# Optimization experiments

Measured on AMD Instinct MI355X. Metric: run time of the kernel, lower is better.

The kernel has to match this reference:

```python
import jax, jax.numpy as jnp
import numpy as np

B, N, D = 16, 512, 12
HID, HEADS = 32, 4
C = HID // HEADS  # per-head channels = 8


def setup_inputs() -> dict:
    key = jax.random.key(0)
    ks = jax.random.split(key, 12)
    s = 0.1
    return {
        "x": jax.random.normal(ks[0], (B, N, D), dtype=jnp.float32),
        "adj": jax.random.randint(ks[1], (B, N, N), 0, 2, dtype=jnp.int32),
        # node_proj: Linear(D, HID)
        "Wp": jax.random.normal(ks[2], (HID, D), dtype=jnp.float32) * s,
        "bp": jax.random.normal(ks[3], (HID,), dtype=jnp.float32) * s,
        # GATConv lin: Linear(HID, HEADS*C, bias=False)
        "Wg": jax.random.normal(ks[4], (HEADS * C, HID), dtype=jnp.float32) * s,
        "att_src": jax.random.normal(ks[5], (HEADS, C), dtype=jnp.float32) * s,
        "att_dst": jax.random.normal(ks[6], (HEADS, C), dtype=jnp.float32) * s,
        "bias_g": jax.random.normal(ks[7], (HEADS * C,), dtype=jnp.float32) * s,
        # edge_mlp: Linear(2*HID, HID) -> ReLU -> Linear(HID, 1) -> Sigmoid
        "W1": jax.random.normal(ks[8], (HID, 2 * HID), dtype=jnp.float32) * s,
        "b1": jax.random.normal(ks[9], (HID,), dtype=jnp.float32) * s,
        "w2": jax.random.normal(ks[10], (HID,), dtype=jnp.float32) * s,
        "b2": jax.random.normal(ks[11], (1,), dtype=jnp.float32) * s,
    }


def reference(x, adj, Wp, bp, Wg, att_src, att_dst, bias_g, W1, b1, w2, b2):
    Bq, Nq, _ = x.shape
    adj_b = adj != 0
    eye = jnp.eye(Nq, dtype=bool)

    # node_proj + ReLU
    h = jax.nn.relu(jnp.einsum('bnd,hd->bnh', x, Wp) + bp)  # [B,N,HID]

    # GATConv (PyG semantics): messages flow src=i (row) -> dst=j (col),
    # self-loops removed then re-added => diagonal forced on.
    g = jnp.einsum('bnd,kd->bnk', h, Wg).reshape(Bq, Nq, HEADS, C)  # [B,N,H,C]
    a_s = jnp.einsum('bnhc,hc->bnh', g, att_src)  # [B,N,H]
    a_d = jnp.einsum('bnhc,hc->bnh', g, att_dst)  # [B,N,H]
    logits = jax.nn.leaky_relu(a_s[:, :, None, :] + a_d[:, None, :, :], 0.2)  # [B,i,j,H]
    mask_sl = adj_b | eye
    logits = jnp.where(mask_sl[..., None], logits, -1e9)
    alpha = jax.nn.softmax(logits, axis=1)  # softmax over source i per target j
    h_gnn = jnp.einsum('bijh,bihc->bjhc', alpha, g).reshape(Bq, Nq, HEADS * C) + bias_g

    # edge MLP on all (i,j) pairs: cat([h_i, h_j]) -> split W1
    W1i, W1j = W1[:, :HID], W1[:, HID:]
    ti = jnp.einsum('bnd,hd->bnh', h_gnn, W1i)  # [B,N,HID] (row / i part)
    tj = jnp.einsum('bnd,hd->bnh', h_gnn, W1j)  # [B,N,HID] (col / j part)
    hidden = jax.nn.relu(ti[:, :, None, :] + tj[:, None, :, :] + b1)  # [B,N,N,HID]
    score = jax.nn.sigmoid(jnp.einsum('bijh,h->bij', hidden, w2) + b2[0])

    out_mask = adj_b & ~eye
    return jnp.where(out_mask, score, jnp.float32(0.0))
```

## Files before the change

### kernel.cpp

```cpp
#include <hip/hip_runtime.h>
#include <cstdint>

#define Bq 16
#define Nq 512
#define Dq 12
#define HID 32
#define HEADS 4
#define Cq 8

#define OFF_G     0u
#define OFF_AS    262144u
#define OFF_AD    294912u
#define OFF_TIT   327680u
#define OFF_TJBT  589824u
#define OFF_PACK  851968u

__global__ __launch_bounds__(256) void k0_node(
    const float* __restrict__ x, const float* __restrict__ Wp, const float* __restrict__ bp,
    const float* __restrict__ Wg, const float* __restrict__ att_src,
    const float* __restrict__ att_dst, float* __restrict__ ws) {
    __shared__ float xs[8 * Dq];
    __shared__ float hs[8][HID];
    int n_sub = threadIdx.x >> 5;
    int k = threadIdx.x & 31;
    int node0 = blockIdx.x * 8;
    if (threadIdx.x < 8 * Dq) xs[threadIdx.x] = x[(size_t)node0 * Dq + threadIdx.x];
    __syncthreads();
    float s = bp[k];
#pragma unroll
    for (int d = 0; d < Dq; d++) s = fmaf(Wp[k * Dq + d], xs[n_sub * Dq + d], s);
    hs[n_sub][k] = s > 0.f ? s : 0.f;
    __syncthreads();
    float g = 0.f;
#pragma unroll
    for (int d = 0; d < HID; d++) g = fmaf(Wg[k * HID + d], hs[n_sub][d], g);
    int nid = node0 + n_sub;
    ws[OFF_G + (size_t)nid * HID + k] = g;
    float ss = g * att_src[k];
    float sd = g * att_dst[k];
#pragma unroll
    for (int off = 1; off < 8; off <<= 1) {
        ss += __shfl_xor(ss, off);
        sd += __shfl_xor(sd, off);
    }
    if ((k & 7) == 0) {
        int h = k >> 3;
        ws[OFF_AS + (size_t)nid * HEADS + h] = ss;
        ws[OFF_AD + (size_t)nid * HEADS + h] = sd;
    }
}

__global__ __launch_bounds__(256, 4) void k1_fused(
    const int* __restrict__ adj, const float* __restrict__ bias_g,
    const float* __restrict__ W1, const float* __restrict__ b1,
    float* __restrict__ ws) {
    int b = blockIdx.y;
    int j0 = blockIdx.x * 8;
    int t = threadIdx.x;
    int jl = t & 7;
    int ig = t >> 3;
    int par = ig >> 4;
    int j = j0 + jl;

    __shared__ float smem[5376];
    float* red = smem;
    float* hgs = smem + 1440;
    float* W1s = smem + 1728;
    float* tjs = smem + 3904;
    uint32_t* mskp = (uint32_t*)(smem + 5120);

    float4 adv = *(const float4*)(ws + OFF_AD + ((size_t)b * Nq + j) * HEADS);
    const float* Gb = ws + OFF_G + (size_t)b * Nq * HID;
    const float* Ab = ws + OFF_AS + (size_t)b * Nq * HEADS;
    int ii_s = t >> 2, q_s = t & 3;

    float4 ga, gb2;
    float av;
    {
        const float* src = Gb + (size_t)ii_s * HID + q_s * 8;
        ga = *(const float4*)src;
        gb2 = *(const float4*)(src + 4);
        av = Ab[t];
        *(float4*)&smem[ii_s * 36 + q_s * 8] = ga;
        *(float4*)&smem[ii_s * 36 + q_s * 8 + 4] = gb2;
        smem[4608 + t] = av;
    }
    const int* adjp = adj + ((size_t)b * Nq + ig) * Nq + j;
    int cur[2], nxt[2];
    cur[0] = adjp[0];
    cur[1] = adjp[(size_t)32 * Nq];

    float lsum[HEADS] = {0.f, 0.f, 0.f, 0.f};
    float acc[HEADS][Cq] = {};
    uint32_t mask = 0;

    for (int c = 0; c < 8; c++) {
        __syncthreads();
        const float* gsc = (c & 1) ? smem + 2304 : smem;
        const float* asc = (c & 1) ? smem + 4864 : smem + 4608;
        if (c < 7) {
            const float* src = Gb + (size_t)((c + 1) * 64 + ii_s) * HID + q_s * 8;
            ga = *(const float4*)src;
            gb2 = *(const float4*)(src + 4);
            av = Ab[(c + 1) * 256 + t];
            nxt[0] = adjp[(size_t)(64 * (c + 1)) * Nq];
            nxt[1] = adjp[(size_t)(64 * (c + 1) + 32) * Nq];
        }
#pragma unroll
        for (int kk = 0; kk < 2; kk++) {
            int i = 64 * c + 32 * kk + ig;
            int a = cur[kk];
            bool msk = (a != 0) || (i == j);
            mask |= (uint32_t)(a != 0) << (4 * c + 2 * kk + par);
            int ii = 32 * kk + ig;
            float4 asv = *(const float4*)&asc[ii * 4];
            const float* gr = &gsc[ii * 36];
            float zs[HEADS] = {asv.x + adv.x, asv.y + adv.y, asv.z + adv.z, asv.w + adv.w};
#pragma unroll
            for (int h = 0; h < HEADS; h++) {
                float z = zs[h];
                float lk = z > 0.f ? z : 0.2f * z;
                float e = msk ? __expf(lk) : 0.f;
                lsum[h] += e;
                float4 g0 = *(const float4*)(gr + h * 8);
                float4 g1 = *(const float4*)(gr + h * 8 + 4);
                acc[h][0] = fmaf(e, g0.x, acc[h][0]);
                acc[h][1] = fmaf(e, g0.y, acc[h][1]);
                acc[h][2] = fmaf(e, g0.z, acc[h][2]);
                acc[h][3] = fmaf(e, g0.w, acc[h][3]);
                acc[h][4] = fmaf(e, g1.x, acc[h][4]);
                acc[h][5] = fmaf(e, g1.y, acc[h][5]);
                acc[h][6] = fmaf(e, g1.z, acc[h][6]);
                acc[h][7] = fmaf(e, g1.w, acc[h][7]);
            }
        }
        if (c < 7) {
            float* gsn = (c & 1) ? smem : smem + 2304;
            float* asn = (c & 1) ? smem + 4608 : smem + 4864;
            *(float4*)&gsn[ii_s * 36 + q_s * 8] = ga;
            *(float4*)&gsn[ii_s * 36 + q_s * 8 + 4] = gb2;
            asn[t] = av;
            cur[0] = nxt[0];
            cur[1] = nxt[1];
        }
    }

    mskp[par * 128 + jl * 16 + (ig & 15)] = mask;

    __syncthreads();

    if (t < 128) {
        int jj = t >> 4, w = t & 15;
        uint32_t word = mskp[jj * 16 + w] | mskp[128 + jj * 16 + w];
        ((uint32_t*)(ws + OFF_PACK))[((size_t)b * Nq + j0 + jj) * 16 + w] = word;
    }
    {
        const float4* src = (const float4*)W1;
        for (int k = t; k < 512; k += 256) {
            int h = k >> 4, q = k & 15;
            *(float4*)&W1s[h * 68 + q * 4] = src[k];
        }
    }
    int w = t >> 6;
    auto dump = [&](int r, float v) {
        v += __shfl_xor(v, 8);
        v += __shfl_xor(v, 16);
        v += __shfl_xor(v, 32);
        if ((t & 63) < 8) red[(r * 8 + jl) * 5 + w] = v;
    };
#pragma unroll
    for (int h = 0; h < HEADS; h++) dump(h, lsum[h]);
#pragma unroll
    for (int h = 0; h < HEADS; h++)
#pragma unroll
        for (int cc = 0; cc < Cq; cc++) dump(4 + h * 8 + cc, acc[h][cc]);
    __syncthreads();
    for (int o = t; o < 288; o += 256) {
        float* pp = &red[o * 5];
        pp[4] = (pp[0] + pp[1]) + (pp[2] + pp[3]);
    }
    __syncthreads();
    {
        int d = t >> 3, jj = t & 7;
        float s = red[((4 + d) * 8 + jj) * 5 + 4];
        float l = red[((d >> 3) * 8 + jj) * 5 + 4];
        hgs[jj * 36 + d] = s * __builtin_amdgcn_rcpf(l) + bias_g[d];
    }
    __syncthreads();
    {
        int tg = t >> 3;
        float si = 0.f, sj = 0.f;
        const float* w0 = &W1s[tg * 68];
        const float* hr = &hgs[jl * 36];
#pragma unroll
        for (int d = 0; d < HID; d++) {
            float hv = hr[d];
            si = fmaf(hv, w0[d], si);
            sj = fmaf(hv, w0[32 + d], sj);
        }
        ws[OFF_TIT + ((size_t)b * HID + tg) * Nq + j] = si;
        tjs[tg * 9 + jl] = sj + b1[tg];
    }
    __syncthreads();
    {
        int jj = t >> 5, h = t & 31;
        ws[OFF_TJBT + ((size_t)b * Nq + j0 + jj) * HID + h] = tjs[h * 9 + jj];
    }
}

__global__ __launch_bounds__(256, 4) void k3_score(const float* __restrict__ w2_p,
                                                   const float* __restrict__ b2_p,
                                                   const float* __restrict__ ws,
                                                   float* __restrict__ out) {
    int b = blockIdx.y;
    int i0 = blockIdx.x * 8;
    int j = threadIdx.x;
    __shared__ float tisT[8 * 36];
    {
        int h = threadIdx.x >> 3, ii = threadIdx.x & 7;
        tisT[ii * 36 + h] = ws[OFF_TIT + ((size_t)b * HID + h) * Nq + i0 + ii];
    }
    float4 ta[8], tb[8];
    const float* rA = ws + OFF_TJBT + ((size_t)b * Nq + j) * HID;
    const float* rB = rA + (size_t)256 * HID;
#pragma unroll
    for (int q = 0; q < 8; q++) {
        ta[q] = *(const float4*)(rA + q * 4);
        tb[q] = *(const float4*)(rB + q * 4);
    }
    float w2l[HID];
#pragma unroll
    for (int h = 0; h < HID; h++) w2l[h] = w2_p[h];
    float b2 = b2_p[0];
    const uint32_t* mrow = (const uint32_t*)(ws + OFF_PACK)
                         + ((size_t)b * Nq + j) * 16 + (i0 & 8);
    uint4 mAv[2], mBv[2];
#pragma unroll
    for (int q = 0; q < 2; q++) {
        mAv[q] = ((const uint4*)mrow)[q];
        mBv[q] = ((const uint4*)(mrow + 256 * 16))[q];
    }
    int bit = i0 >> 4;
    __syncthreads();
#pragma unroll
    for (int ii = 0; ii < 8; ii++) {
        int i = i0 + ii;
        uint32_t mA = (ii & 3) == 0 ? mAv[ii >> 2].x : (ii & 3) == 1 ? mAv[ii >> 2].y
                    : (ii & 3) == 2 ? mAv[ii >> 2].z : mAv[ii >> 2].w;
        uint32_t mB = (ii & 3) == 0 ? mBv[ii >> 2].x : (ii & 3) == 1 ? mBv[ii >> 2].y
                    : (ii & 3) == 2 ? mBv[ii >> 2].z : mBv[ii >> 2].w;
        bool onA = (((mA >> bit) & 1u) != 0) && (i != j);
        bool onB = (((mB >> bit) & 1u) != 0) && (i != j + 256);
        float sA = b2, sB = b2;
#pragma unroll
        for (int q = 0; q < 8; q++) {
            float4 tq = *(const float4*)&tisT[ii * 36 + q * 4];
#pragma unroll
            for (int e = 0; e < 4; e++) {
                float ti = (e == 0) ? tq.x : (e == 1) ? tq.y : (e == 2) ? tq.z : tq.w;
                float tjA = (e == 0) ? ta[q].x : (e == 1) ? ta[q].y : (e == 2) ? ta[q].z : ta[q].w;
                float tjB = (e == 0) ? tb[q].x : (e == 1) ? tb[q].y : (e == 2) ? tb[q].z : tb[q].w;
                float tA = ti + tjA;
                tA = tA > 0.f ? tA : 0.f;
                sA = fmaf(tA, w2l[q * 4 + e], sA);
                float tB = ti + tjB;
                tB = tB > 0.f ? tB : 0.f;
                sB = fmaf(tB, w2l[q * 4 + e], sB);
            }
        }
        float scA = __builtin_amdgcn_rcpf(1.f + __expf(-sA));
        float scB = __builtin_amdgcn_rcpf(1.f + __expf(-sB));
        out[((size_t)b * Nq + i) * Nq + j] = onA ? scA : 0.f;
        out[((size_t)b * Nq + i) * Nq + j + 256] = onB ? scB : 0.f;
    }
}

extern "C" void kernel_launch(void* const* d_in, const int* in_sizes, int n_in,
                              void* d_out, int out_size, void* d_ws, size_t ws_size,
                              hipStream_t stream) {
    const float* x       = (const float*)d_in[0];
    const int*   adj     = (const int*)d_in[1];
    const float* Wp      = (const float*)d_in[2];
    const float* bp      = (const float*)d_in[3];
    const float* Wg      = (const float*)d_in[4];
    const float* att_src = (const float*)d_in[5];
    const float* att_dst = (const float*)d_in[6];
    const float* bias_g  = (const float*)d_in[7];
    const float* W1      = (const float*)d_in[8];
    const float* b1      = (const float*)d_in[9];
    const float* w2      = (const float*)d_in[10];
    const float* b2      = (const float*)d_in[11];
    float* out = (float*)d_out;
    float* ws = (float*)d_ws;
    (void)in_sizes; (void)n_in; (void)out_size; (void)ws_size;

    k0_node<<<dim3(1024), dim3(256), 0, stream>>>(x, Wp, bp, Wg, att_src, att_dst, ws);
    k1_fused<<<dim3(Nq / 8, Bq), dim3(256), 0, stream>>>(adj, bias_g, W1, b1, ws);
    k3_score<<<dim3(64, Bq), dim3(256), 0, stream>>>(w2, b2, ws, out);
}
```

Measured before the change: 133.4 us.

## Read node features directly from global memory and prefetch all adjacency into registers

```diff
diff --git a/kernel.cpp b/kernel.cpp
--- a/kernel.cpp
+++ b/kernel.cpp
@@ -7,6 +7,7 @@
 #define HID 32
 #define HEADS 4
 #define Cq 8
+#define LOG2E 1.44269504088896f
 
 #define OFF_G     0u
 #define OFF_AS    262144u
@@ -45,8 +46,8 @@
     }
     if ((k & 7) == 0) {
         int h = k >> 3;
-        ws[OFF_AS + (size_t)nid * HEADS + h] = ss;
-        ws[OFF_AD + (size_t)nid * HEADS + h] = sd;
+        ws[OFF_AS + (size_t)nid * HEADS + h] = ss * LOG2E;
+        ws[OFF_AD + (size_t)nid * HEADS + h] = sd * LOG2E;
     }
 }
 
@@ -62,86 +63,59 @@
     int par = ig >> 4;
     int j = j0 + jl;
 
-    __shared__ float smem[5376];
+    __shared__ float smem[4448];
     float* red = smem;
     float* hgs = smem + 1440;
     float* W1s = smem + 1728;
     float* tjs = smem + 3904;
-    uint32_t* mskp = (uint32_t*)(smem + 5120);
+    uint32_t* mskp = (uint32_t*)(smem + 4192);
 
     float4 adv = *(const float4*)(ws + OFF_AD + ((size_t)b * Nq + j) * HEADS);
     const float* Gb = ws + OFF_G + (size_t)b * Nq * HID;
     const float* Ab = ws + OFF_AS + (size_t)b * Nq * HEADS;
-    int ii_s = t >> 2, q_s = t & 3;
-
-    float4 ga, gb2;
-    float av;
-    {
-        const float* src = Gb + (size_t)ii_s * HID + q_s * 8;
-        ga = *(const float4*)src;
-        gb2 = *(const float4*)(src + 4);
-        av = Ab[t];
-        *(float4*)&smem[ii_s * 36 + q_s * 8] = ga;
-        *(float4*)&smem[ii_s * 36 + q_s * 8 + 4] = gb2;
-        smem[4608 + t] = av;
-    }
+
+    {
+        const float4* src = (const float4*)W1;
+        for (int k = t; k < 512; k += 256) {
+            int h = k >> 4, q = k & 15;
+            *(float4*)&W1s[h * 68 + q * 4] = src[k];
+        }
+    }
+
     const int* adjp = adj + ((size_t)b * Nq + ig) * Nq + j;
-    int cur[2], nxt[2];
-    cur[0] = adjp[0];
-    cur[1] = adjp[(size_t)32 * Nq];
+    int areg[16];
+#pragma unroll
+    for (int m = 0; m < 16; m++) areg[m] = adjp[(size_t)(32 * m) * Nq];
 
     float lsum[HEADS] = {0.f, 0.f, 0.f, 0.f};
     float acc[HEADS][Cq] = {};
     uint32_t mask = 0;
 
-    for (int c = 0; c < 8; c++) {
-        __syncthreads();
-        const float* gsc = (c & 1) ? smem + 2304 : smem;
-        const float* asc = (c & 1) ? smem + 4864 : smem + 4608;
-        if (c < 7) {
-            const float* src = Gb + (size_t)((c + 1) * 64 + ii_s) * HID + q_s * 8;
-            ga = *(const float4*)src;
-            gb2 = *(const float4*)(src + 4);
-            av = Ab[(c + 1) * 256 + t];
-            nxt[0] = adjp[(size_t)(64 * (c + 1)) * Nq];
-            nxt[1] = adjp[(size_t)(64 * (c + 1) + 32) * Nq];
-        }
-#pragma unroll
-        for (int kk = 0; kk < 2; kk++) {
-            int i = 64 * c + 32 * kk + ig;
-            int a = cur[kk];
-            bool msk = (a != 0) || (i == j);
-            mask |= (uint32_t)(a != 0) << (4 * c + 2 * kk + par);
-            int ii = 32 * kk + ig;
-            float4 asv = *(const float4*)&asc[ii * 4];
-            const float* gr = &gsc[ii * 36];
-            float zs[HEADS] = {asv.x + adv.x, asv.y + adv.y, asv.z + adv.z, asv.w + adv.w};
-#pragma unroll
-            for (int h = 0; h < HEADS; h++) {
-                float z = zs[h];
-                float lk = z > 0.f ? z : 0.2f * z;
-                float e = msk ? __expf(lk) : 0.f;
-                lsum[h] += e;
-                float4 g0 = *(const float4*)(gr + h * 8);
-                float4 g1 = *(const float4*)(gr + h * 8 + 4);
-                acc[h][0] = fmaf(e, g0.x, acc[h][0]);
-                acc[h][1] = fmaf(e, g0.y, acc[h][1]);
-                acc[h][2] = fmaf(e, g0.z, acc[h][2]);
-                acc[h][3] = fmaf(e, g0.w, acc[h][3]);
-                acc[h][4] = fmaf(e, g1.x, acc[h][4]);
-                acc[h][5] = fmaf(e, g1.y, acc[h][5]);
-                acc[h][6] = fmaf(e, g1.z, acc[h][6]);
-                acc[h][7] = fmaf(e, g1.w, acc[h][7]);
-            }
-        }
-        if (c < 7) {
-            float* gsn = (c & 1) ? smem : smem + 2304;
-            float* asn = (c & 1) ? smem + 4608 : smem + 4864;
-            *(float4*)&gsn[ii_s * 36 + q_s * 8] = ga;
-            *(float4*)&gsn[ii_s * 36 + q_s * 8 + 4] = gb2;
-            asn[t] = av;
-            cur[0] = nxt[0];
-            cur[1] = nxt[1];
+#pragma unroll 2
+    for (int m = 0; m < 16; m++) {
+        int i = 32 * m + ig;
+        bool on = (areg[m] != 0);
+        bool msk = on || (i == j);
+        mask |= (uint32_t)on << (2 * m + par);
+        float4 asv = *(const float4*)(Ab + (size_t)i * HEADS);
+        const float4* gr4 = (const float4*)(Gb + (size_t)i * HID);
+        float zs[HEADS] = {asv.x + adv.x, asv.y + adv.y, asv.z + adv.z, asv.w + adv.w};
+#pragma unroll
+        for (int h = 0; h < HEADS; h++) {
+            float z = zs[h];
+            float lk = fmaxf(z, 0.2f * z);
+            float e = msk ? __builtin_amdgcn_exp2f(lk) : 0.f;
+            lsum[h] += e;
+            float4 g0 = gr4[2 * h];
+            float4 g1 = gr4[2 * h + 1];
+            acc[h][0] = fmaf(e, g0.x, acc[h][0]);
+            acc[h][1] = fmaf(e, g0.y, acc[h][1]);
+            acc[h][2] = fmaf(e, g0.z, acc[h][2]);
+            acc[h][3] = fmaf(e, g0.w, acc[h][3]);
+            acc[h][4] = fmaf(e, g1.x, acc[h][4]);
+            acc[h][5] = fmaf(e, g1.y, acc[h][5]);
+            acc[h][6] = fmaf(e, g1.z, acc[h][6]);
+            acc[h][7] = fmaf(e, g1.w, acc[h][7]);
         }
     }
 
@@ -153,13 +127,6 @@
         int jj = t >> 4, w = t & 15;
         uint32_t word = mskp[jj * 16 + w] | mskp[128 + jj * 16 + w];
         ((uint32_t*)(ws + OFF_PACK))[((size_t)b * Nq + j0 + jj) * 16 + w] = word;
-    }
-    {
-        const float4* src = (const float4*)W1;
-        for (int k = t; k < 512; k += 256) {
-            int h = k >> 4, q = k & 15;
-            *(float4*)&W1s[h * 68 + q * 4] = src[k];
-        }
     }
     int w = t >> 6;
     auto dump = [&](int r, float v) {
```

New measurement: 145.3 us. 8.9% more time.
